# Performance work log

Hardware: AMD Instinct MI355X
Metric: run time of the kernel (lower is better)

The kernel has to match this reference:

```python
import jax, jax.numpy as jnp
import numpy as np

H = 512   # d_model
NH = 32   # N // 2
LVAL = 8192

def setup_inputs() -> dict:
    key = jax.random.key(0)
    k1, k2, k3, k4, k5 = jax.random.split(key, 5)
    import math
    # log_dt ~ U[log(0.001), log(0.1)] as in the torch init
    log_dt = jax.random.uniform(k1, (H,), dtype=jnp.float32) * (math.log(0.1) - math.log(0.001)) + math.log(0.001)
    log_A_real = jax.random.normal(k2, (H, NH), dtype=jnp.float32)
    A_imag = jax.random.normal(k3, (H, NH), dtype=jnp.float32)
    B = jax.random.normal(k4, (H, NH, 2), dtype=jnp.float32)
    C = jax.random.normal(k5, (H, NH, 2), dtype=jnp.float32) * 0.004
    return {"log_dt": log_dt, "log_A_real": log_A_real, "A_imag": A_imag, "B": B, "C": C, "L": LVAL}

def reference(log_dt, log_A_real, A_imag, B, C, L):
    dt = jnp.exp(log_dt)                                  # (H,)
    A = -jnp.exp(log_A_real) - 1j * A_imag                # (H, Nh) complex64, Re(A) < 0
    Bc = B[..., 0] + 1j * B[..., 1]                       # (H, Nh)
    Cc = C[..., 0] + 1j * C[..., 1]                       # (H, Nh)
    dtA = A * dt[:, None]                                 # (H, Nh)
    # Vandermonde tensor: exp(dtA * l) for l in [0, L)
    K = jnp.exp(dtA[:, :, None] * jnp.arange(L, dtype=jnp.float32))  # (H, Nh, L)
    Ceff = Bc * Cc * (jnp.exp(dtA) - 1.0) / A             # (H, Nh)
    out = 2.0 * jnp.real(jnp.einsum('hn,hnl->hl', Ceff, K))  # (H, L)
    return out
```

## Files before the change

### kernel.cpp

```cpp
#include <hip/hip_runtime.h>
#include <math.h>

#define HDIM 512
#define NH   32
#define LTOT 8192
#define CHUNK 8
#define TPB  256
#define BANDL  512

typedef float v2f __attribute__((ext_vector_type(2)));

__global__ __launch_bounds__(TPB, 8) void s4_kernel(
    const float* __restrict__ log_dt,
    const float* __restrict__ log_A_real,
    const float* __restrict__ A_imag,
    const float* __restrict__ Bmat,
    const float* __restrict__ Cmat,
    float* __restrict__ out)
{
    __shared__ float4 p0[NH];
    __shared__ float4 p1[NH];
    __shared__ float4 p2[NH];

    const int bid  = blockIdx.x;
    const int h    = bid & (HDIM - 1);
    const int q    = bid >> 9;
    const int tid  = threadIdx.x;

    if (tid < NH) {
        const int n   = tid;
        const int idx = h * NH + n;
        const float dt = expf(log_dt[h]);
        const float Ar = -expf(log_A_real[idx]);
        const float Ai = -A_imag[idx];
        const float re = Ar * dt;
        const float im = Ai * dt;
        float sw, cw;
        sincosf(im, &sw, &cw);
        const float er = expf(re);
        const float wr = er * cw;
        const float wi = er * sw;
        const float inv = 1.0f / (Ar * Ar + Ai * Ai);
        const float nr = wr - 1.0f, ni = wi;
        const float qr = (nr * Ar + ni * Ai) * inv;
        const float qi = (ni * Ar - nr * Ai) * inv;
        const float Br = Bmat[2 * idx], Bi = Bmat[2 * idx + 1];
        const float Cr = Cmat[2 * idx], Ci = Cmat[2 * idx + 1];
        const float bcr = Br * Cr - Bi * Ci;
        const float bci = Br * Ci + Bi * Cr;
        const float e0r = 2.0f * (bcr * qr - bci * qi);
        const float e0i = 2.0f * (bcr * qi + bci * qr);
        const float e1r = e0r * wr - e0i * wi, e1i = e0r * wi + e0i * wr;
        const float e2r = e1r * wr - e1i * wi, e2i = e1r * wi + e1i * wr;
        const float e3r = e2r * wr - e2i * wi, e3i = e2r * wi + e2i * wr;
        const float b1 = er * er;

        const float key = re * 1.44269504089f;
        int rank = 0;
#pragma unroll
        for (int m = 0; m < NH; ++m) {
            const float km = __shfl(key, m, 64);
            rank += (km > key || (km == key && m < n)) ? 1 : 0;
        }
        p0[rank] = make_float4(key, im * 0.15915494309f,
                               2.0f * (wr * wr - wi * wi), b1 * b1);
        p1[rank] = make_float4(e0r, e1r, e0i, e1i);
        p2[rank] = make_float4(e2r, e3r, e2i, e3i);
    }
    __syncthreads();

    const int wave = tid >> 6;
    const int lane = tid & 63;
    const int band = wave * 4 + q;
    const int l0   = band * BANDL + lane * CHUNK;
    const float l0f    = (float)l0;
    const float l0minf = (float)(band * BANDL);

    v2f acc2[CHUNK / 2];
#pragma unroll
    for (int k = 0; k < CHUNK / 2; ++k) acc2[k] = v2f{0.0f, 0.0f};

#pragma unroll 1
    for (int n = 0; n < NH; ++n) {
        const float4 P0 = p0[n];
        if (P0.x * l0minf < -17.3f) break;
        const float4 Q1 = p1[n];
        const float4 Q2 = p2[n];
        float ph = P0.y * l0f;
        ph = __builtin_amdgcn_fractf(ph);
        const float s = __builtin_amdgcn_sinf(ph);
        const float c = __builtin_amdgcn_cosf(ph);
        const float e = __builtin_amdgcn_exp2f(P0.x * l0f);
        const float kr = e * c;
        const float ki = e * s;
        v2f Pa = v2f{Q1.x, Q1.y} * kr - v2f{Q1.z, Q1.w} * ki;
        v2f Pb = v2f{Q2.x, Q2.y} * kr - v2f{Q2.z, Q2.w} * ki;
        acc2[0] += Pa;
        acc2[1] += Pb;
        const v2f a2 = v2f{P0.z, P0.z};
        const v2f b2 = v2f{P0.w, P0.w};
#pragma unroll
        for (int k = 2; k < CHUNK / 2; ++k) {
            const v2f Pn = a2 * Pb - b2 * Pa;
            acc2[k] += Pn;
            Pa = Pb;
            Pb = Pn;
        }
    }

    float4* o = (float4*)(out + (size_t)h * LTOT + l0);
#pragma unroll
    for (int j = 0; j < CHUNK / 4; ++j)
        o[j] = make_float4(acc2[2 * j].x, acc2[2 * j].y,
                           acc2[2 * j + 1].x, acc2[2 * j + 1].y);
}

extern "C" void kernel_launch(void* const* d_in, const int* in_sizes, int n_in,
                              void* d_out, int out_size, void* d_ws, size_t ws_size,
                              hipStream_t stream)
{
    (void)in_sizes; (void)n_in; (void)d_ws; (void)ws_size; (void)out_size;
    const float* log_dt     = (const float*)d_in[0];
    const float* log_A_real = (const float*)d_in[1];
    const float* A_imag     = (const float*)d_in[2];
    const float* Bmat       = (const float*)d_in[3];
    const float* Cmat       = (const float*)d_in[4];
    float* out = (float*)d_out;

    s4_kernel<<<dim3(HDIM * 4), dim3(TPB), 0, stream>>>(
        log_dt, log_A_real, A_imag, Bmat, Cmat, out);
}
```

Measured before the change: 84.14 us.

## Split per-mode parameter setup into separate kernel via workspace

Moves the per-(h,n) parameter computation and sorting into a small preceding kernel that writes sorted float4 parameters to the workspace. The main kernel then only loads 96 float4s into shared memory instead of having 32 threads do transcendental setup while the rest of the block waits. This avoids repeating the setup in each of the four blocks per h, at the cost of an extra kernel launch and a global round trip. If no workspace is provided, it falls back to the original monolithic kernel.

```diff
diff --git a/kernel.cpp b/kernel.cpp
--- a/kernel.cpp
+++ b/kernel.cpp
@@ -7,10 +7,136 @@
 #define CHUNK 8
 #define TPB  256
 #define BANDL  512
+#define WS_BYTES (HDIM * 96 * 16)
 
 typedef float v2f __attribute__((ext_vector_type(2)));
 
-__global__ __launch_bounds__(TPB, 8) void s4_kernel(
+
+__device__ __forceinline__ void compute_params(
+    int h, int n, const float* log_dt, const float* log_A_real,
+    const float* A_imag, const float* Bmat, const float* Cmat,
+    float4& P0, float4& P1, float4& P2, float& key)
+{
+    const int idx = h * NH + n;
+    const float dt = expf(log_dt[h]);
+    const float Ar = -expf(log_A_real[idx]);
+    const float Ai = -A_imag[idx];
+    const float re = Ar * dt;
+    const float im = Ai * dt;
+    float sw, cw;
+    sincosf(im, &sw, &cw);
+    const float er = expf(re);
+    const float wr = er * cw;
+    const float wi = er * sw;
+    const float inv = 1.0f / (Ar * Ar + Ai * Ai);
+    const float nr = wr - 1.0f, ni = wi;
+    const float qr = (nr * Ar + ni * Ai) * inv;
+    const float qi = (ni * Ar - nr * Ai) * inv;
+    const float Br = Bmat[2 * idx], Bi = Bmat[2 * idx + 1];
+    const float Cr = Cmat[2 * idx], Ci = Cmat[2 * idx + 1];
+    const float bcr = Br * Cr - Bi * Ci;
+    const float bci = Br * Ci + Bi * Cr;
+    const float e0r = 2.0f * (bcr * qr - bci * qi);
+    const float e0i = 2.0f * (bcr * qi + bci * qr);
+    const float e1r = e0r * wr - e0i * wi, e1i = e0r * wi + e0i * wr;
+    const float e2r = e1r * wr - e1i * wi, e2i = e1r * wi + e1i * wr;
+    const float e3r = e2r * wr - e2i * wi, e3i = e2r * wi + e2i * wr;
+    const float b1 = er * er;
+    key = re * 1.44269504089f;
+    P0 = make_float4(key, im * 0.15915494309f,
+                     2.0f * (wr * wr - wi * wi), b1 * b1);
+    P1 = make_float4(e0r, e1r, e0i, e1i);
+    P2 = make_float4(e2r, e3r, e2i, e3i);
+}
+
+__global__ __launch_bounds__(TPB) void s4_params(
+    const float* __restrict__ log_dt,
+    const float* __restrict__ log_A_real,
+    const float* __restrict__ A_imag,
+    const float* __restrict__ Bmat,
+    const float* __restrict__ Cmat,
+    float4* __restrict__ ws)
+{
+    const int idx = blockIdx.x * TPB + threadIdx.x;
+    const int h = idx >> 5;
+    const int n = idx & 31;
+    float4 P0, P1, P2;
+    float key;
+    compute_params(h, n, log_dt, log_A_real, A_imag, Bmat, Cmat,
+                   P0, P1, P2, key);
+    int rank = 0;
+#pragma unroll
+    for (int m = 0; m < 32; ++m) {
+        const float km = __shfl(key, m, 32);
+        rank += (km > key || (km == key && m < n)) ? 1 : 0;
+    }
+    float4* base = ws + h * 96;
+    base[rank]      = P0;
+    base[32 + rank] = P1;
+    base[64 + rank] = P2;
+}
+
+__global__ __launch_bounds__(TPB, 8) void s4_main(
+    const float4* __restrict__ ws,
+    float* __restrict__ out)
+{
+    __shared__ float4 sp[96];
+
+    const int bid  = blockIdx.x;
+    const int h    = bid & (HDIM - 1);
+    const int q    = bid >> 9;
+    const int tid  = threadIdx.x;
+
+    if (tid < 96) sp[tid] = ws[h * 96 + tid];
+    __syncthreads();
+
+    const int wave = tid >> 6;
+    const int lane = tid & 63;
+    const int band = wave * 4 + q;
+    const int l0   = band * BANDL + lane * CHUNK;
+    const float l0f    = (float)l0;
+    const float l0minf = (float)(band * BANDL);
+
+    v2f acc2[CHUNK / 2];
+#pragma unroll
+    for (int k = 0; k < CHUNK / 2; ++k) acc2[k] = v2f{0.0f, 0.0f};
+
+#pragma unroll 1
+    for (int n = 0; n < NH; ++n) {
+        const float4 P0 = sp[n];
+        if (P0.x * l0minf < -17.3f) break;
+        const float4 Q1 = sp[32 + n];
+        const float4 Q2 = sp[64 + n];
+        float ph = P0.y * l0f;
+        ph = __builtin_amdgcn_fractf(ph);
+        const float s = __builtin_amdgcn_sinf(ph);
+        const float c = __builtin_amdgcn_cosf(ph);
+        const float e = __builtin_amdgcn_exp2f(P0.x * l0f);
+        const float kr = e * c;
+        const float ki = e * s;
+        v2f Pa = v2f{Q1.x, Q1.y} * kr - v2f{Q1.z, Q1.w} * ki;
+        v2f Pb = v2f{Q2.x, Q2.y} * kr - v2f{Q2.z, Q2.w} * ki;
+        acc2[0] += Pa;
+        acc2[1] += Pb;
+        const v2f a2 = v2f{P0.z, P0.z};
+        const v2f b2 = v2f{P0.w, P0.w};
+#pragma unroll
+        for (int k = 2; k < CHUNK / 2; ++k) {
+            const v2f Pn = a2 * Pb - b2 * Pa;
+            acc2[k] += Pn;
+            Pa = Pb;
+            Pb = Pn;
+        }
+    }
+
+    float4* o = (float4*)(out + (size_t)h * LTOT + l0);
+#pragma unroll
+    for (int j = 0; j < CHUNK / 4; ++j)
+        o[j] = make_float4(acc2[2 * j].x, acc2[2 * j].y,
+                           acc2[2 * j + 1].x, acc2[2 * j + 1].y);
+}
+
+__global__ __launch_bounds__(TPB, 8) void s4_kernel_mono(
     const float* __restrict__ log_dt,
     const float* __restrict__ log_A_real,
     const float* __restrict__ A_imag,
@@ -28,44 +154,18 @@
     const int tid  = threadIdx.x;
 
     if (tid < NH) {
-        const int n   = tid;
-        const int idx = h * NH + n;
-        const float dt = expf(log_dt[h]);
-        const float Ar = -expf(log_A_real[idx]);
-        const float Ai = -A_imag[idx];
-        const float re = Ar * dt;
-        const float im = Ai * dt;
-        float sw, cw;
-        sincosf(im, &sw, &cw);
-        const float er = expf(re);
-        const float wr = er * cw;
-        const float wi = er * sw;
-        const float inv = 1.0f / (Ar * Ar + Ai * Ai);
-        const float nr = wr - 1.0f, ni = wi;
-        const float qr = (nr * Ar + ni * Ai) * inv;
-        const float qi = (ni * Ar - nr * Ai) * inv;
-        const float Br = Bmat[2 * idx], Bi = Bmat[2 * idx + 1];
-        const float Cr = Cmat[2 * idx], Ci = Cmat[2 * idx + 1];
-        const float bcr = Br * Cr - Bi * Ci;
-        const float bci = Br * Ci + Bi * Cr;
-        const float e0r = 2.0f * (bcr * qr - bci * qi);
-        const float e0i = 2.0f * (bcr * qi + bci * qr);
-        const float e1r = e0r * wr - e0i * wi, e1i = e0r * wi + e0i * wr;
-        const float e2r = e1r * wr - e1i * wi, e2i = e1r * wi + e1i * wr;
-        const float e3r = e2r * wr - e2i * wi, e3i = e2r * wi + e2i * wr;
-        const float b1 = er * er;
-
-        const float key = re * 1.44269504089f;
+        const int n = tid;
+        float4 P0, P1, P2;
+        float key;
+        compute_params(h, n, log_dt, log_A_real, A_imag, Bmat, Cmat,
+                       P0, P1, P2, key);
         int rank = 0;
 #pragma unroll
         for (int m = 0; m < NH; ++m) {
             const float km = __shfl(key, m, 64);
             rank += (km > key || (km == key && m < n)) ? 1 : 0;
         }
-        p0[rank] = make_float4(key, im * 0.15915494309f,
-                               2.0f * (wr * wr - wi * wi), b1 * b1);
-        p1[rank] = make_float4(e0r, e1r, e0i, e1i);
-        p2[rank] = make_float4(e2r, e3r, e2i, e3i);
+        p0[rank] = P0; p1[rank] = P1; p2[rank] = P2;
     }
     __syncthreads();
 
@@ -119,7 +219,7 @@
                               void* d_out, int out_size, void* d_ws, size_t ws_size,
                               hipStream_t stream)
 {
-    (void)in_sizes; (void)n_in; (void)d_ws; (void)ws_size; (void)out_size;
+    (void)in_sizes; (void)n_in; (void)out_size;
     const float* log_dt     = (const float*)d_in[0];
     const float* log_A_real = (const float*)d_in[1];
     const float* A_imag     = (const float*)d_in[2];
@@ -127,6 +227,13 @@
     const float* Cmat       = (const float*)d_in[4];
     float* out = (float*)d_out;
 
-    s4_kernel<<<dim3(HDIM * 4), dim3(TPB), 0, stream>>>(
-        log_dt, log_A_real, A_imag, Bmat, Cmat, out);
-}
+    if (d_ws != nullptr && ws_size >= (size_t)WS_BYTES) {
+        float4* ws = (float4*)d_ws;
+        s4_params<<<dim3(HDIM * NH / TPB), dim3(TPB), 0, stream>>>(
+            log_dt, log_A_real, A_imag, Bmat, Cmat, ws);
+        s4_main<<<dim3(HDIM * 4), dim3(TPB), 0, stream>>>(ws, out);
+    } else {
+        s4_kernel_mono<<<dim3(HDIM * 4), dim3(TPB), 0, stream>>>(
+            log_dt, log_A_real, A_imag, Bmat, Cmat, out);
+    }
+}
```

Measured after the change: 85.63 us. Within noise of the previous version (+1.8%).
